# Optimization experiments

Measured on AMD Instinct MI355X. Metric: run time of the kernel, lower is better.

## Reference

```python
import jax, jax.numpy as jnp
import numpy as np

T_TOK, N_UNITS, E, H, L_PATH, N_PATHS, B, VOCAB = 16, 4096, 128, 128, 32, 1024, 8, 16384
MAX_PATH_LEN = 32
PAD_ID = 0


def _run_lstm(x, Wi, Wh, b):
    # x: [T, N, E]; torch gate order i, f, g, o
    Hh = Wh.shape[1]
    h0 = jnp.zeros((x.shape[1], Hh), x.dtype)
    def step(carry, xt):
        h, c = carry
        g = xt @ Wi.T + h @ Wh.T + b
        i, f, gg, o = jnp.split(g, 4, axis=-1)
        c = jax.nn.sigmoid(f) * c + jax.nn.sigmoid(i) * jnp.tanh(gg)
        h = jax.nn.sigmoid(o) * jnp.tanh(c)
        return (h, c), h
    _, ys = jax.lax.scan(step, (h0, h0), x)
    return ys


def _bilstm(x, lengths, Wif, Whf, bf, Wib, Whb, bb):
    # emulates pack_padded_sequence + bidirectional LSTM + pad_packed (zeros past length)
    T = x.shape[0]
    t = jnp.arange(T)[:, None]
    valid = t < lengths[None, :]
    out_f = _run_lstm(x, Wif, Whf, bf)
    rev = jnp.clip(lengths[None, :] - 1 - t, 0, T - 1)  # reverse within each valid prefix
    x_rev = jnp.take_along_axis(x, rev[:, :, None], axis=0)
    out_b = jnp.take_along_axis(_run_lstm(x_rev, Wib, Whb, bb), rev[:, :, None], axis=0)
    return jnp.concatenate([out_f, out_b], axis=-1) * valid[:, :, None]


def _layernorm(x, g, b):
    m = x.mean(-1, keepdims=True)
    v = ((x - m) ** 2).mean(-1, keepdims=True)
    return (x - m) * jax.lax.rsqrt(v + 1e-5) * g + b


def _forward(units, paths, unit_per_data, path_per_data, emb, tl_Wif, tl_Whf, tl_bf,
             tl_Wib, tl_Whb, tl_bb, lin_W, lin_b, ln_g, ln_b, attn_w, attn_b,
             pl_Wif, pl_Whf, pl_bf, pl_Wib, pl_Whb, pl_bb, ul_W, ul_b):
    # ---- _token_encoder ----
    is_pad = units == PAD_ID
    tok_len = jnp.where(is_pad.any(0), jnp.argmax(is_pad, 0), units.shape[0])
    x = emb[units]                                              # [T, NU, E]
    h = _bilstm(x, tok_len, tl_Wif, tl_Whf, tl_bf, tl_Wib, tl_Whb, tl_bb)  # [T, NU, 2H]
    out = h @ lin_W.T + lin_b                                   # [T, NU, E]
    q = jnp.tanh(_layernorm(out, ln_g, ln_b))
    scores = q @ attn_w.T + attn_b                              # [T, NU, 1] local attention
    scores = jnp.where(is_pad[:, :, None], -1e9, scores)
    w = jax.nn.softmax(scores, axis=0)
    tok_feat = jnp.einsum('tn,tne->ne', w[..., 0], out)         # [NU, E]
    # ---- _unit_to_path (vectorized ragged gather) ----
    Lp, Pn = paths.shape
    has_end = (paths == -1).any(0)
    fe = jnp.where(has_end, jnp.argmax(paths == -1, 0), Lp)
    ML = min(Lp, MAX_PATH_LEN)
    nb = unit_per_data.shape[0]
    data_of_path = jnp.repeat(jnp.arange(nb), path_per_data, total_repeat_length=Pn)
    u_off = jnp.cumsum(unit_per_data) - unit_per_data
    off_p = u_off[data_of_path]
    un_p = unit_per_data[data_of_path]
    pL = paths[:ML]
    t = jnp.arange(ML)[:, None]
    within = t < fe[None, :]
    keep = within & (pL >= 0) & (pL < un_p[None, :])
    gidx = jnp.clip(jnp.clip(pL, 0, None) + off_p[None, :], 0, tok_feat.shape[0] - 1)
    feats = tok_feat[gidx] * keep[:, :, None]                   # [ML, P, E]
    mask = jnp.where(within, (pL < 0) | (pL > un_p[None, :]), True)
    # ---- _path_encoder ----
    p_len = jnp.where(mask.any(0), jnp.argmax(mask, 0), ML)
    hp = _bilstm(feats, p_len, pl_Wif, pl_Whf, pl_bf, pl_Wib, pl_Whb, pl_bb)
    return hp @ ul_W.T + ul_b                                   # [ML, P, E]


def setup_inputs() -> dict:
    rng = np.random.default_rng(0)
    tok_len = rng.integers(4, T_TOK + 1, N_UNITS); tok_len[0] = T_TOK
    units = rng.integers(1, VOCAB, (T_TOK, N_UNITS))
    units = np.where(np.arange(T_TOK)[:, None] < tok_len[None, :], units, PAD_ID)
    upd = N_UNITS // B
    p_len = rng.integers(8, L_PATH + 1, N_PATHS); p_len[0] = L_PATH
    paths = rng.integers(0, upd, (L_PATH, N_PATHS))
    paths = np.where(np.arange(L_PATH)[:, None] < p_len[None, :], paths, -1)
    key = jax.random.key(0)
    ks = iter(jax.random.split(key, 24))
    def pn(shape, s=0.08):
        return (jax.random.normal(next(ks), shape) * s).astype(jnp.float32)
    return dict(
        units=jnp.asarray(units, jnp.int32),
        paths=jnp.asarray(paths, jnp.int32),
        unit_per_data=jnp.full((B,), upd, jnp.int32),
        path_per_data=jnp.full((B,), N_PATHS // B, jnp.int32),
        emb=pn((VOCAB, E)),
        tl_Wif=pn((4 * H, E)), tl_Whf=pn((4 * H, H)), tl_bf=pn((4 * H,)),
        tl_Wib=pn((4 * H, E)), tl_Whb=pn((4 * H, H)), tl_bb=pn((4 * H,)),
        lin_W=pn((E, 2 * H)), lin_b=pn((E,)),
        ln_g=jnp.ones((E,), jnp.float32), ln_b=jnp.zeros((E,), jnp.float32),
        attn_w=pn((1, E)), attn_b=pn((1,)),
        pl_Wif=pn((4 * H, E)), pl_Whf=pn((4 * H, H)), pl_bf=pn((4 * H,)),
        pl_Wib=pn((4 * H, E)), pl_Whb=pn((4 * H, H)), pl_bb=pn((4 * H,)),
        ul_W=pn((E, 2 * H)), ul_b=pn((E,)),
    )


def reference(units, paths, unit_per_data, path_per_data, emb, tl_Wif, tl_Whf, tl_bf,
              tl_Wib, tl_Whb, tl_bb, lin_W, lin_b, ln_g, ln_b, attn_w, attn_b,
              pl_Wif, pl_Whf, pl_bf, pl_Wib, pl_Whb, pl_bb, ul_W, ul_b):
    return _forward(units, paths, unit_per_data, path_per_data, emb, tl_Wif, tl_Whf, tl_bf,
                    tl_Wib, tl_Whb, tl_bb, lin_W, lin_b, ln_g, ln_b, attn_w, attn_b,
                    pl_Wif, pl_Whf, pl_bf, pl_Wib, pl_Whb, pl_bb, ul_W, ul_b)
```

## Files before the change

### kernel.cpp

```cpp
#include <hip/hip_runtime.h>
#include <cstdint>
#include <cstddef>

#define T_TOKN 16
#define NUNITS 4096
#define LPATH  32
#define NPATHS 1024
#define BNUM   8

typedef __attribute__((ext_vector_type(8))) short short8;
typedef __attribute__((ext_vector_type(4))) short short4x;
typedef __attribute__((ext_vector_type(4))) float f32x4;

enum : size_t {
  OFF_WFRAG   = 0,
  OFF_LINFRAG = 262144,
  OFF_OUTF    = 294912,
  OFF_OUTB    = OFF_OUTF + 4194304,
  OFF_OUTLIN  = OFF_OUTB + 4194304,
  OFF_SCORES  = OFF_OUTLIN + 8388608,
  OFF_TOKFEAT = OFF_SCORES + 65536,
  OFF_POUTF   = OFF_TOKFEAT + 524288,
  OFF_POUTB   = OFF_POUTF + 2097152,
  OFF_INT     = OFF_POUTB + 2097152,
  WS_FLOATS   = OFF_INT + 8192
};

static __device__ __forceinline__ unsigned short f2bf(float f) {
  union { float f; unsigned u; } v; v.f = f;
  unsigned r = v.u + 0x7fffu + ((v.u >> 16) & 1u);
  return (unsigned short)(r >> 16);
}
static __device__ __forceinline__ unsigned pack_bf(float a, float b) {
  return (unsigned)f2bf(a) | ((unsigned)f2bf(b) << 16);
}
static __device__ __forceinline__ float sigf(float x)      { return 1.f / (1.f + __expf(-x)); }
static __device__ __forceinline__ float tanhfast(float x)  { return 2.f / (1.f + __expf(-2.f * x)) - 1.f; }

__global__ void prep_kernel(
    const float* __restrict__ tWif, const float* __restrict__ tWhf,
    const float* __restrict__ tWib, const float* __restrict__ tWhb,
    const float* __restrict__ pWif, const float* __restrict__ pWhf,
    const float* __restrict__ pWib, const float* __restrict__ pWhb,
    const float* __restrict__ linW, const float* __restrict__ ulW,
    const int* __restrict__ units, const int* __restrict__ paths,
    const int* __restrict__ upd, const int* __restrict__ ppd,
    float* __restrict__ ws, int* __restrict__ ip)
{
  int idx = blockIdx.x * 256 + threadIdx.x;
  if (idx < 524288) {
    unsigned short* wf = (unsigned short*)(ws + OFF_WFRAG);
    int mat = idx >> 17, rem = idx & 131071;
    int i  = rem & 7;
    int lane = (rem >> 3) & 63;
    int ct = (rem >> 9) & 3;
    int ks = (rem >> 11) & 7;
    int wv = (rem >> 14) & 7;
    int g = wv * 64 + ct * 16 + (lane & 15);
    int k = ks * 32 + ((lane >> 4) << 3) + i;
    const float* Wi; const float* Wh;
    switch (mat) {
      case 0: Wi = tWif; Wh = tWhf; break;
      case 1: Wi = tWib; Wh = tWhb; break;
      case 2: Wi = pWif; Wh = pWhf; break;
      default: Wi = pWib; Wh = pWhb; break;
    }
    float v = (k < 128) ? Wi[g * 128 + k] : Wh[g * 128 + (k - 128)];
    wf[idx] = f2bf(v);
  } else if (idx < 524288 + 65536) {
    unsigned short* lf = (unsigned short*)(ws + OFF_LINFRAG);
    int i2 = idx - 524288;
    int mat = i2 >> 15, rem = i2 & 32767;
    int i  = rem & 7;
    int lane = (rem >> 3) & 63;
    int ks = (rem >> 9) & 7;
    int ct = (rem >> 12) & 7;
    int e = ct * 16 + (lane & 15);
    int k = ks * 32 + ((lane >> 4) << 3) + i;
    const float* W = mat ? ulW : linW;
    lf[i2] = f2bf(W[e * 256 + k]);
  } else if (idx < 589824 + 4096) {
    int n = idx - 589824;
    int len = T_TOKN;
    for (int t = 0; t < T_TOKN; ++t)
      if (units[t * NUNITS + n] == 0) { len = t; break; }
    ip[n] = len;
  } else if (idx < 589824 + 5120) {
    int p = idx - (589824 + 4096);
    int* fe_a  = ip + 4096;
    int* p_len = ip + 5120;
    int* off_p = ip + 6144;
    int* un_p  = ip + 7168;
    int cum = 0; int d = BNUM - 1;
    for (int dd = 0; dd < BNUM; ++dd) {
      int c2 = cum + ppd[dd];
      if (p < c2) { d = dd; break; }
      cum = c2;
    }
    int off = 0;
    for (int dd = 0; dd < d; ++dd) off += upd[dd];
    int un = upd[d];
    off_p[p] = off; un_p[p] = un;
    int f = LPATH;
    for (int t = 0; t < LPATH; ++t)
      if (paths[t * NPATHS + p] == -1) { f = t; break; }
    fe_a[p] = f;
    int pl = LPATH;
    for (int t = 0; t < LPATH; ++t) {
      int v = paths[t * NPATHS + p];
      if ((t >= f) || (v < 0) || (v > un)) { pl = t; break; }
    }
    p_len[p] = pl;
  }
}

template <int MODE>
__global__ __launch_bounds__(1024, 4) void lstm_kernel(
    const unsigned short* __restrict__ wfragAll,
    const float* __restrict__ biasF, const float* __restrict__ biasB,
    const float* __restrict__ src,
    const int* __restrict__ idxsrc,
    const int* __restrict__ lens,
    const int* __restrict__ fe_a, const int* __restrict__ off_p, const int* __restrict__ un_p,
    unsigned short* __restrict__ outF, unsigned short* __restrict__ outB)
{
  constexpr int NN   = MODE ? NPATHS : NUNITS;
  constexpr int TT   = MODE ? LPATH : T_TOKN;
  constexpr int M    = MODE ? 8 : 32;
  constexpr int MR   = MODE ? 16 : 32;
  constexpr int NRT  = MR / 16;
  constexpr int ASTR = 264;
  constexpr int GSTR = 514;

  __shared__ unsigned short ash[MR * ASTR];
  __shared__ float gates[MR * GSTR];

  int tid  = threadIdx.x;
  int dir  = blockIdx.y;
  int n0   = blockIdx.x * M;
  int lane = tid & 63, wv = tid >> 6;

  const unsigned short* wbase =
      wfragAll + (size_t)((MODE ? 2 : 0) + dir) * 131072;
  int wv8 = wv >> 1;
  short8 bfr[8][2];
#pragma unroll
  for (int ks = 0; ks < 8; ++ks)
#pragma unroll
    for (int c2 = 0; c2 < 2; ++c2) {
      int ct = ((wv & 1) << 1) | c2;
      bfr[ks][c2] = *(const short8*)&wbase[((((wv8 * 8 + ks) * 4 + ct) * 64) + lane) * 8];
    }

  if (MODE == 0) {
    for (int i = tid; i < MR * 128; i += 1024)
      ash[(i >> 7) * ASTR + 128 + (i & 127)] = 0;
  } else {
    for (int i = tid; i < MR * ASTR; i += 1024) ash[i] = 0;
  }

  const float* bcp = dir ? biasB : biasF;
  int j2 = MODE ? (tid & 127) : ((tid & 63) * 2);
  int ug = MODE ? (tid >> 7)  : (tid >> 6);
  float2 b2[4];
#pragma unroll
  for (int q = 0; q < 4; ++q) {
    if (MODE == 0) b2[q] = *(const float2*)&bcp[q * 128 + j2];
    else           b2[q] = make_float2(bcp[q * 128 + j2], 0.f);
  }
  constexpr int NU = MODE ? 1 : 2;
  float cst0[NU], cst1[NU];
  int   ulen[NU];
#pragma unroll
  for (int i = 0; i < NU; ++i) {
    cst0[i] = 0.f; cst1[i] = 0.f;
    ulen[i] = lens[n0 + ug * NU + i];
  }

  int gu, gk0;
  if (MODE == 0) { gu = tid >> 5; gk0 = (tid & 31) * 4; }
  else           { gu = tid >> 7; gk0 = tid & 127; }
  int gn = n0 + gu;
  int glen = lens[gn];
  int gfe = 0, goff = 0, gun = 0;
  if (MODE) { gfe = fe_a[gn]; goff = off_p[gn]; gun = un_p[gn]; }

  float4 xq; float xs;
  if (MODE == 0) {
    int tau = dir ? min(max(glen - 1, 0), TT - 1) : 0;
    int tok = idxsrc[tau * NN + gn];
    xq = *(const float4*)&src[(size_t)tok * 128 + gk0];
  } else {
    int tau = dir ? min(max(glen - 1, 0), TT - 1) : 0;
    int v = idxsrc[tau * NN + gn];
    bool keep = (tau < gfe) && (v >= 0) && (v < gun);
    xs = 0.f;
    if (keep) xs = src[(size_t)min(v + goff, NUNITS - 1) * 128 + gk0];
  }
  __syncthreads();

  for (int t = 0; t < TT; ++t) {
    if (MODE == 0) {
      short4x x4;
      x4[0] = (short)f2bf(xq.x); x4[1] = (short)f2bf(xq.y);
      x4[2] = (short)f2bf(xq.z); x4[3] = (short)f2bf(xq.w);
      *(short4x*)&ash[gu * ASTR + gk0] = x4;
    } else {
      ash[gu * ASTR + gk0] = f2bf(xs);
    }
    __syncthreads();

    {
      int tn = (t + 1 < TT) ? t + 1 : t;
      int taun = dir ? min(max(glen - 1 - tn, 0), TT - 1) : tn;
      int vn = idxsrc[taun * NN + gn];
      f32x4 acc[NRT][2];
#pragma unroll
      for (int rt = 0; rt < NRT; ++rt)
#pragma unroll
        for (int c2 = 0; c2 < 2; ++c2) {
          f32x4 z = {0.f, 0.f, 0.f, 0.f};
          acc[rt][c2] = z;
        }
#pragma unroll
      for (int ks = 0; ks < 8; ++ks) {
        short8 afr[NRT];
#pragma unroll
        for (int rt = 0; rt < NRT; ++rt)
          afr[rt] = *(const short8*)&ash[(rt * 16 + (lane & 15)) * ASTR + ks * 32 + ((lane >> 4) << 3)];
#pragma unroll
        for (int rt = 0; rt < NRT; ++rt)
#pragma unroll
          for (int c2 = 0; c2 < 2; ++c2)
            acc[rt][c2] = __builtin_amdgcn_mfma_f32_16x16x32_bf16(
                afr[rt], bfr[ks][c2], acc[rt][c2], 0, 0, 0);
      }
      if (MODE == 0) {
        xq = *(const float4*)&src[(size_t)vn * 128 + gk0];
      } else {
        bool keep = (taun < gfe) && (vn >= 0) && (vn < gun);
        xs = 0.f;
        if (keep) xs = src[(size_t)min(vn + goff, NUNITS - 1) * 128 + gk0];
      }
#pragma unroll
      for (int rt = 0; rt < NRT; ++rt)
#pragma unroll
        for (int c2 = 0; c2 < 2; ++c2) {
          int g = wv * 32 + c2 * 16 + (lane & 15);
#pragma unroll
          for (int r = 0; r < 4; ++r) {
            int u = rt * 16 + ((lane >> 4) << 2) + r;
            gates[u * GSTR + g] = acc[rt][c2][r];
          }
        }
    }
    __syncthreads();

#pragma unroll
    for (int i = 0; i < NU; ++i) {
      int u = ug * NU + i;
      int n = n0 + u;
      if (MODE == 0) {
        float2 g0 = *(const float2*)&gates[u * GSTR + j2];
        float2 g1 = *(const float2*)&gates[u * GSTR + 128 + j2];
        float2 g2 = *(const float2*)&gates[u * GSTR + 256 + j2];
        float2 g3 = *(const float2*)&gates[u * GSTR + 384 + j2];
        float i0 = sigf(g0.x + b2[0].x), i1 = sigf(g0.y + b2[0].y);
        float f0 = sigf(g1.x + b2[1].x), f1 = sigf(g1.y + b2[1].y);
        float c0 = tanhfast(g2.x + b2[2].x), c1 = tanhfast(g2.y + b2[2].y);
        float o0 = sigf(g3.x + b2[3].x), o1 = sigf(g3.y + b2[3].y);
        float cA = f0 * cst0[i] + i0 * c0;
        float cB = f1 * cst1[i] + i1 * c1;
        cst0[i] = cA; cst1[i] = cB;
        float h0 = o0 * tanhfast(cA);
        float h1 = o1 * tanhfast(cB);
        unsigned hp = pack_bf(h0, h1);
        *(unsigned*)&ash[u * ASTR + 128 + j2] = hp;
        if (dir == 0) {
          *(unsigned*)&outF[((size_t)t * NN + n) * 128 + j2] = hp;
        } else {
          int L = ulen[i];
          if (t < L) *(unsigned*)&outB[((size_t)(L - 1 - t) * NN + n) * 128 + j2] = hp;
          else       *(unsigned*)&outB[((size_t)t * NN + n) * 128 + j2] = 0;
        }
      } else {
        float p0 = gates[u * GSTR + j2]       + b2[0].x;
        float p1 = gates[u * GSTR + 128 + j2] + b2[1].x;
        float p2 = gates[u * GSTR + 256 + j2] + b2[2].x;
        float p3 = gates[u * GSTR + 384 + j2] + b2[3].x;
        float ig = sigf(p0), fg = sigf(p1), gg = tanhfast(p2), og = sigf(p3);
        float c = fg * cst0[i] + ig * gg;
        cst0[i] = c;
        float h = og * tanhfast(c);
        unsigned short hb = f2bf(h);
        ash[u * ASTR + 128 + j2] = hb;
        if (dir == 0) {
          outF[((size_t)t * NN + n) * 128 + j2] = hb;
        } else {
          int L = ulen[i];
          if (t < L) outB[((size_t)(L - 1 - t) * NN + n) * 128 + j2] = hb;
          else       outB[((size_t)t * NN + n) * 128 + j2] = 0;
        }
      }
    }
  }
}

template <int EPI>
__global__ __launch_bounds__(256) void gemm_mfma(
    const unsigned short* __restrict__ INf, const unsigned short* __restrict__ INb,
    const int* __restrict__ lens,
    const unsigned short* __restrict__ Bfrag, const float* __restrict__ bias,
    float* __restrict__ OUT, float* __restrict__ scores,
    const float* __restrict__ lng, const float* __restrict__ lnb,
    const float* __restrict__ attw, const float* __restrict__ attb,
    const int* __restrict__ units, int Nn)
{
  constexpr int OSTR = 132;
  __shared__ float outs[64 * OSTR];
  __shared__ float red1[256];
  __shared__ float red2[256];
  __shared__ float rowm[64], rowr[64];
  __shared__ float awsh[128], lgsh[128], lbsh[128];

  int tid = threadIdx.x, lane = tid & 63, wv = tid >> 6;
  int row0 = blockIdx.x * 64;
  int t = row0 / Nn, n0 = row0 % Nn;

  if (EPI == 1 && tid < 128) {
    awsh[tid] = attw[tid]; lgsh[tid] = lng[tid]; lbsh[tid] = lnb[tid];
  }

  short8 bfr[8][2];
#pragma unroll
  for (int ks = 0; ks < 8; ++ks)
#pragma unroll
    for (int c2 = 0; c2 < 2; ++c2) {
      int ct = wv * 2 + c2;
      bfr[ks][c2] = *(const short8*)&Bfrag[(((ct * 8 + ks) * 64) + lane) * 8];
    }

  int rb = lane & 15;
  int koq = (lane >> 4) << 3;
  bool val[4];
#pragma unroll
  for (int rt = 0; rt < 4; ++rt)
    val[rt] = (EPI == 1) ? true : (t < lens[n0 + rt * 16 + rb]);

  f32x4 acc[4][2];
#pragma unroll
  for (int rt = 0; rt < 4; ++rt)
#pragma unroll
    for (int c2 = 0; c2 < 2; ++c2) {
      f32x4 z = {0.f, 0.f, 0.f, 0.f};
      acc[rt][c2] = z;
    }

#pragma unroll
  for (int ks = 0; ks < 8; ++ks) {
    const unsigned short* P = (ks < 4) ? INf : INb;
    int koff = (ks & 3) * 32 + koq;
#pragma unroll
    for (int rt = 0; rt < 4; ++rt) {
      short8 a = {0, 0, 0, 0, 0, 0, 0, 0};
      if (val[rt])
        a = *(const short8*)&P[((size_t)(row0 + rt * 16 + rb)) * 128 + koff];
#pragma unroll
      for (int c2 = 0; c2 < 2; ++c2)
        acc[rt][c2] = __builtin_amdgcn_mfma_f32_16x16x32_bf16(
            a, bfr[ks][c2], acc[rt][c2], 0, 0, 0);
    }
  }

  float bc[2];
#pragma unroll
  for (int c2 = 0; c2 < 2; ++c2) bc[c2] = bias[wv * 32 + c2 * 16 + rb];
#pragma unroll
  for (int rt = 0; rt < 4; ++rt)
#pragma unroll
    for (int c2 = 0; c2 < 2; ++c2) {
      int col = wv * 32 + c2 * 16 + rb;
      int ub  = rt * 16 + ((lane >> 4) << 2);
#pragma unroll
      for (int r = 0; r < 4; ++r)
        outs[(ub + r) * OSTR + col] = acc[rt][c2][r] + bc[c2];
    }
  __syncthreads();

  int row = tid >> 2, seg = tid & 3;
  const float* rp = &outs[row * OSTR + seg * 32];
  size_t go = ((size_t)(row0 + row)) * 128 + seg * 32;

  if (EPI == 0) {
#pragma unroll
    for (int x = 0; x < 8; ++x)
      *(f32x4*)&OUT[go + x * 4] = *(const f32x4*)&rp[x * 4];
  } else {
    f32x4 v[8];
    float s = 0.f, s2 = 0.f;
#pragma unroll
    for (int x = 0; x < 8; ++x) {
      v[x] = *(const f32x4*)&rp[x * 4];
#pragma unroll
      for (int c = 0; c < 4; ++c) { s += v[x][c]; s2 += v[x][c] * v[x][c]; }
    }
    red1[tid] = s; red2[tid] = s2;
    __syncthreads();
    if (tid < 64) {
      float a = red1[tid * 4] + red1[tid * 4 + 1] + red1[tid * 4 + 2] + red1[tid * 4 + 3];
      float b = red2[tid * 4] + red2[tid * 4 + 1] + red2[tid * 4 + 2] + red2[tid * 4 + 3];
      float m = a * (1.f / 128.f);
      float var = b * (1.f / 128.f) - m * m;
      rowm[tid] = m;
      rowr[tid] = rsqrtf(var + 1e-5f);
    }
    __syncthreads();
    float m = rowm[row], rs = rowr[row];
    float sp = 0.f;
#pragma unroll
    for (int x = 0; x < 8; ++x) {
#pragma unroll
      for (int c = 0; c < 4; ++c) {
        int col = seg * 32 + x * 4 + c;
        float q = tanhfast((v[x][c] - m) * rs * lgsh[col] + lbsh[col]);
        sp += q * awsh[col];
      }
      *(f32x4*)&OUT[go + x * 4] = v[x];
    }
    red1[tid] = sp;
    __syncthreads();
    if (tid < 64) {
      float s3 = red1[tid * 4] + red1[tid * 4 + 1] + red1[tid * 4 + 2] + red1[tid * 4 + 3]
               + attb[0];
      int n = n0 + tid;
      if (units[t * NUNITS + n] == 0) s3 = -1e9f;
      scores[t * NUNITS + n] = s3;
    }
  }
}

__global__ __launch_bounds__(128) void softmax_feat_kernel(
    const float* __restrict__ scores, const float* __restrict__ out_lin,
    float* __restrict__ tok_feat)
{
  int n = blockIdx.x;
  int e = threadIdx.x;
  float s[T_TOKN];
  float m = -1e30f;
#pragma unroll
  for (int t = 0; t < T_TOKN; ++t) { s[t] = scores[t * NUNITS + n]; m = fmaxf(m, s[t]); }
  float sum = 0.f;
#pragma unroll
  for (int t = 0; t < T_TOKN; ++t) { s[t] = expf(s[t] - m); sum += s[t]; }
  float inv = 1.f / sum;
  float a = 0.f;
#pragma unroll
  for (int t = 0; t < T_TOKN; ++t)
    a += s[t] * inv * out_lin[((size_t)t * NUNITS + n) * 128 + e];
  tok_feat[n * 128 + e] = a;
}

extern "C" void kernel_launch(void* const* d_in, const int* in_sizes, int n_in,
                              void* d_out, int out_size, void* d_ws, size_t ws_size,
                              hipStream_t stream)
{
  const int*   units = (const int*)d_in[0];
  const int*   paths = (const int*)d_in[1];
  const int*   upd   = (const int*)d_in[2];
  const int*   ppd   = (const int*)d_in[3];
  const float* emb   = (const float*)d_in[4];
  const float* tWif  = (const float*)d_in[5];
  const float* tWhf  = (const float*)d_in[6];
  const float* tbf   = (const float*)d_in[7];
  const float* tWib  = (const float*)d_in[8];
  const float* tWhb  = (const float*)d_in[9];
  const float* tbb   = (const float*)d_in[10];
  const float* linW  = (const float*)d_in[11];
  const float* linb  = (const float*)d_in[12];
  const float* lng   = (const float*)d_in[13];
  const float* lnb   = (const float*)d_in[14];
  const float* attw  = (const float*)d_in[15];
  const float* attb  = (const float*)d_in[16];
  const float* pWif  = (const float*)d_in[17];
  const float* pWhf  = (const float*)d_in[18];
  const float* pbf   = (const float*)d_in[19];
  const float* pWib  = (const float*)d_in[20];
  const float* pWhb  = (const float*)d_in[21];
  const float* pbb   = (const float*)d_in[22];
  const float* ulW   = (const float*)d_in[23];
  const float* ulb   = (const float*)d_in[24];

  float* ws = (float*)d_ws;
  int*   ip = (int*)(ws + OFF_INT);
  if (ws_size < WS_FLOATS * sizeof(float)) return;

  unsigned short* wfrag   = (unsigned short*)(ws + OFF_WFRAG);
  unsigned short* linfrag = (unsigned short*)(ws + OFF_LINFRAG);
  unsigned short* ulfrag  = linfrag + 32768;
  unsigned short* OUTF  = (unsigned short*)(ws + OFF_OUTF);
  unsigned short* OUTB  = (unsigned short*)(ws + OFF_OUTB);
  unsigned short* POUTF = (unsigned short*)(ws + OFF_POUTF);
  unsigned short* POUTB = (unsigned short*)(ws + OFF_POUTB);

  prep_kernel<<<2324, 256, 0, stream>>>(tWif, tWhf, tWib, tWhb,
                                        pWif, pWhf, pWib, pWhb,
                                        linW, ulW, units, paths, upd, ppd,
                                        ws, ip);

  lstm_kernel<0><<<dim3(128, 2), 1024, 0, stream>>>(
      wfrag, tbf, tbb, emb, units, ip , nullptr, nullptr, nullptr,
      OUTF, OUTB);

  gemm_mfma<1><<<1024, 256, 0, stream>>>(
      OUTF, OUTB, ip , linfrag, linb,
      ws + OFF_OUTLIN, ws + OFF_SCORES, lng, lnb, attw, attb, units, NUNITS);

  softmax_feat_kernel<<<4096, 128, 0, stream>>>(ws + OFF_SCORES, ws + OFF_OUTLIN,
                                                ws + OFF_TOKFEAT);

  lstm_kernel<1><<<dim3(128, 2), 1024, 0, stream>>>(
      wfrag, pbf, pbb, ws + OFF_TOKFEAT, paths, ip + 5120 ,
      ip + 4096 , ip + 6144 , ip + 7168 ,
      POUTF, POUTB);

  gemm_mfma<0><<<512, 256, 0, stream>>>(
      POUTF, POUTB, ip + 5120 , ulfrag, ulb,
      (float*)d_out, nullptr, nullptr, nullptr, nullptr, nullptr, nullptr, NPATHS);
}
```

Measured before the change: 322.2 us.

## Ping-pong two row groups in LSTM so pointwise overlaps the other group's MFMA

The LSTM recurrence kernel now splits each block's rows into two independent groups of 16 with double-buffered shared A-tiles and gate buffers. The MFMA step for one group is interleaved with the pointwise gate update of the other, so each barrier phase mixes matrix and elementwise work instead of running them serially. It also skips the gate math for padded timesteps and just writes zeros. The cost is more complex control flow and extra shared memory. Mode 1 now leaves half its threads idle in the pointwise phase and clamps the path index.

```diff
diff --git a/kernel.cpp b/kernel.cpp
--- a/kernel.cpp
+++ b/kernel.cpp
@@ -9,7 +9,6 @@
 #define BNUM   8
 
 typedef __attribute__((ext_vector_type(8))) short short8;
-typedef __attribute__((ext_vector_type(4))) short short4x;
 typedef __attribute__((ext_vector_type(4))) float f32x4;
 
 enum : size_t {
@@ -126,19 +125,18 @@
 {
   constexpr int NN   = MODE ? NPATHS : NUNITS;
   constexpr int TT   = MODE ? LPATH : T_TOKN;
-  constexpr int M    = MODE ? 8 : 32;
-  constexpr int MR   = MODE ? 16 : 32;
-  constexpr int NRT  = MR / 16;
+  constexpr int GR   = MODE ? 4 : 16;
   constexpr int ASTR = 264;
   constexpr int GSTR = 514;
 
-  __shared__ unsigned short ash[MR * ASTR];
-  __shared__ float gates[MR * GSTR];
+  __shared__ unsigned short ash[2][16 * ASTR];
+  __shared__ float gates[2][16 * GSTR];
 
   int tid  = threadIdx.x;
   int dir  = blockIdx.y;
-  int n0   = blockIdx.x * M;
+  int n0   = blockIdx.x * (2 * GR);
   int lane = tid & 63, wv = tid >> 6;
+  int koq  = (lane >> 4) << 3;
 
   const unsigned short* wbase =
       wfragAll + (size_t)((MODE ? 2 : 0) + dir) * 131072;
@@ -152,158 +150,163 @@
       bfr[ks][c2] = *(const short8*)&wbase[((((wv8 * 8 + ks) * 4 + ct) * 64) + lane) * 8];
     }
 
-  if (MODE == 0) {
-    for (int i = tid; i < MR * 128; i += 1024)
-      ash[(i >> 7) * ASTR + 128 + (i & 127)] = 0;
-  } else {
-    for (int i = tid; i < MR * ASTR; i += 1024) ash[i] = 0;
+  for (int i = tid; i < 2 * 16 * ASTR / 2; i += 1024) ((unsigned*)ash)[i] = 0u;
+
+  int j2 = MODE ? (tid & 127) : (lane * 2);
+  int ug = MODE ? (tid >> 7) : (tid >> 6);
+
+  int nn[2], ulen[2];
+  int gfe[2] = {0, 0}, goff[2] = {0, 0}, gun[2] = {0, 0};
+#pragma unroll
+  for (int g = 0; g < 2; ++g) {
+    int n = n0 + g * GR + ug;
+    if constexpr (MODE) n = min(n, NPATHS - 1);
+    nn[g] = n; ulen[g] = lens[n];
+    if constexpr (MODE) { gfe[g] = fe_a[n]; goff[g] = off_p[n]; gun[g] = un_p[n]; }
   }
 
   const float* bcp = dir ? biasB : biasF;
-  int j2 = MODE ? (tid & 127) : ((tid & 63) * 2);
-  int ug = MODE ? (tid >> 7)  : (tid >> 6);
   float2 b2[4];
 #pragma unroll
   for (int q = 0; q < 4; ++q) {
-    if (MODE == 0) b2[q] = *(const float2*)&bcp[q * 128 + j2];
-    else           b2[q] = make_float2(bcp[q * 128 + j2], 0.f);
-  }
-  constexpr int NU = MODE ? 1 : 2;
-  float cst0[NU], cst1[NU];
-  int   ulen[NU];
-#pragma unroll
-  for (int i = 0; i < NU; ++i) {
-    cst0[i] = 0.f; cst1[i] = 0.f;
-    ulen[i] = lens[n0 + ug * NU + i];
-  }
-
-  int gu, gk0;
-  if (MODE == 0) { gu = tid >> 5; gk0 = (tid & 31) * 4; }
-  else           { gu = tid >> 7; gk0 = tid & 127; }
-  int gn = n0 + gu;
-  int glen = lens[gn];
-  int gfe = 0, goff = 0, gun = 0;
-  if (MODE) { gfe = fe_a[gn]; goff = off_p[gn]; gun = un_p[gn]; }
-
-  float4 xq; float xs;
-  if (MODE == 0) {
-    int tau = dir ? min(max(glen - 1, 0), TT - 1) : 0;
-    int tok = idxsrc[tau * NN + gn];
-    xq = *(const float4*)&src[(size_t)tok * 128 + gk0];
-  } else {
-    int tau = dir ? min(max(glen - 1, 0), TT - 1) : 0;
-    int v = idxsrc[tau * NN + gn];
-    bool keep = (tau < gfe) && (v >= 0) && (v < gun);
-    xs = 0.f;
-    if (keep) xs = src[(size_t)min(v + goff, NUNITS - 1) * 128 + gk0];
-  }
+    if constexpr (MODE == 0) b2[q] = *(const float2*)&bcp[q * 128 + j2];
+    else                     b2[q] = make_float2(bcp[q * 128 + j2], 0.f);
+  }
+
+  float cst0[2] = {0.f, 0.f}, cst1[2] = {0.f, 0.f};
+  float2 xq2[2];
+  float  xq1[2];
+  (void)xq2; (void)xq1; (void)cst1;
+
+#define XLOAD(GG, TN) do {                                                    \
+    int tc = min((TN), TT - 1);                                               \
+    if constexpr (MODE == 0) {                                                \
+      int tau = dir ? min(max(ulen[GG] - 1 - tc, 0), TT - 1) : tc;            \
+      int tok = idxsrc[tau * NN + nn[GG]];                                    \
+      xq2[GG] = *(const float2*)&src[(size_t)tok * 128 + j2];                 \
+    } else {                                                                  \
+      if (ug < GR) {                                                          \
+        int tau = dir ? min(max(ulen[GG] - 1 - tc, 0), TT - 1) : tc;          \
+        int v = idxsrc[tau * NN + nn[GG]];                                    \
+        bool keep = (tau < gfe[GG]) && (v >= 0) && (v < gun[GG]);             \
+        float xv = 0.f;                                                       \
+        if (keep) xv = src[(size_t)min(v + goff[GG], NUNITS - 1) * 128 + j2]; \
+        xq1[GG] = xv;                                                         \
+      }                                                                       \
+    }                                                                         \
+  } while (0)
+
+#define XWRITE(GG) do {                                                       \
+    if constexpr (MODE == 0)                                                  \
+      *(unsigned*)&ash[GG][ug * ASTR + j2] = pack_bf(xq2[GG].x, xq2[GG].y);   \
+    else if (ug < GR)                                                         \
+      ash[GG][ug * ASTR + j2] = f2bf(xq1[GG]);                                \
+  } while (0)
+
+#define GSTORE(GG, P0, P1) do {                                               \
+    int col = wv * 32 + (lane & 15);                                          \
+    int ub  = (lane >> 4) << 2;                                               \
+    float* gg = gates[GG];                                                    \
+    for (int r = 0; r < 4; ++r) {                                             \
+      gg[(ub + r) * GSTR + col]      = (P0)[r];                               \
+      gg[(ub + r) * GSTR + col + 16] = (P1)[r];                               \
+    }                                                                         \
+  } while (0)
+
+#define POINTWISE(GG, TPW) do {                                               \
+    int tpw = (TPW);                                                          \
+    if constexpr (MODE == 0) {                                                \
+      int L = ulen[GG]; int n = nn[GG];                                       \
+      if (tpw < L) {                                 \
+        const float* gg = gates[GG] + ug * GSTR + j2;                         \
+        float2 g0 = *(const float2*)(gg);                                     \
+        float2 g1 = *(const float2*)(gg + 128);                               \
+        float2 g2 = *(const float2*)(gg + 256);                               \
+        float2 g3 = *(const float2*)(gg + 384);                               \
+        float i0 = sigf(g0.x + b2[0].x), i1 = sigf(g0.y + b2[0].y);           \
+        float f0 = sigf(g1.x + b2[1].x), f1 = sigf(g1.y + b2[1].y);           \
+        float c0 = tanhfast(g2.x + b2[2].x), c1 = tanhfast(g2.y + b2[2].y);   \
+        float o0 = sigf(g3.x + b2[3].x), o1 = sigf(g3.y + b2[3].y);           \
+        float cA = f0 * cst0[GG] + i0 * c0;                                   \
+        float cB = f1 * cst1[GG] + i1 * c1;                                   \
+        cst0[GG] = cA; cst1[GG] = cB;                                         \
+        unsigned hp = pack_bf(o0 * tanhfast(cA), o1 * tanhfast(cB));          \
+        *(unsigned*)&ash[GG][ug * ASTR + 128 + j2] = hp;                      \
+        if (dir == 0)                                                         \
+          *(unsigned*)&outF[((size_t)tpw * NN + n) * 128 + j2] = hp;          \
+        else                                                                  \
+          *(unsigned*)&outB[((size_t)(L - 1 - tpw) * NN + n) * 128 + j2] = hp;\
+      } else {                 \
+        if (dir == 0)                                                         \
+          *(unsigned*)&outF[((size_t)tpw * NN + n) * 128 + j2] = 0u;          \
+        else                                                                  \
+          *(unsigned*)&outB[((size_t)tpw * NN + n) * 128 + j2] = 0u;          \
+      }                                                                       \
+    } else if (ug < GR) {                                                     \
+      int L = ulen[GG]; int n = nn[GG];                                       \
+      if (tpw < L) {                                                          \
+        const float* gg = gates[GG] + ug * GSTR + j2;                         \
+        float p0 = gg[0]   + b2[0].x;                                         \
+        float p1 = gg[128] + b2[1].x;                                         \
+        float p2 = gg[256] + b2[2].x;                                         \
+        float p3 = gg[384] + b2[3].x;                                         \
+        float c = sigf(p1) * cst0[GG] + sigf(p0) * tanhfast(p2);              \
+        cst0[GG] = c;                                                         \
+        unsigned short hb = f2bf(sigf(p3) * tanhfast(c));                     \
+        ash[GG][ug * ASTR + 128 + j2] = hb;                                   \
+        if (dir == 0) outF[((size_t)tpw * NN + n) * 128 + j2] = hb;           \
+        else          outB[((size_t)(L - 1 - tpw) * NN + n) * 128 + j2] = hb; \
+      } else {                                                                \
+        if (dir == 0) outF[((size_t)tpw * NN + n) * 128 + j2] = 0;            \
+        else          outB[((size_t)tpw * NN + n) * 128 + j2] = 0;            \
+      }                                                                       \
+    }                                                                         \
+  } while (0)
+
   __syncthreads();
-
+  XLOAD(0, 0);
+  XLOAD(1, 0);
+  XWRITE(0);
+  __syncthreads();
+
+#pragma unroll 1
   for (int t = 0; t < TT; ++t) {
-    if (MODE == 0) {
-      short4x x4;
-      x4[0] = (short)f2bf(xq.x); x4[1] = (short)f2bf(xq.y);
-      x4[2] = (short)f2bf(xq.z); x4[3] = (short)f2bf(xq.w);
-      *(short4x*)&ash[gu * ASTR + gk0] = x4;
-    } else {
-      ash[gu * ASTR + gk0] = f2bf(xs);
+    {
+      f32x4 p0 = {0.f, 0.f, 0.f, 0.f}, p1 = {0.f, 0.f, 0.f, 0.f};
+#pragma unroll
+      for (int ks = 0; ks < 8; ++ks) {
+        short8 a = *(const short8*)&ash[0][(lane & 15) * ASTR + ks * 32 + koq];
+        p0 = __builtin_amdgcn_mfma_f32_16x16x32_bf16(a, bfr[ks][0], p0, 0, 0, 0);
+        p1 = __builtin_amdgcn_mfma_f32_16x16x32_bf16(a, bfr[ks][1], p1, 0, 0, 0);
+      }
+      XWRITE(1);
+      if (t + 1 < TT) XLOAD(0, t + 1);
+      if (t > 0) POINTWISE(1, t - 1);
+      GSTORE(0, p0, p1);
     }
     __syncthreads();
 
     {
-      int tn = (t + 1 < TT) ? t + 1 : t;
-      int taun = dir ? min(max(glen - 1 - tn, 0), TT - 1) : tn;
-      int vn = idxsrc[taun * NN + gn];
-      f32x4 acc[NRT][2];
-#pragma unroll
-      for (int rt = 0; rt < NRT; ++rt)
-#pragma unroll
-        for (int c2 = 0; c2 < 2; ++c2) {
-          f32x4 z = {0.f, 0.f, 0.f, 0.f};
-          acc[rt][c2] = z;
-        }
+      f32x4 p0 = {0.f, 0.f, 0.f, 0.f}, p1 = {0.f, 0.f, 0.f, 0.f};
 #pragma unroll
       for (int ks = 0; ks < 8; ++ks) {
-        short8 afr[NRT];
-#pragma unroll
-        for (int rt = 0; rt < NRT; ++rt)
-          afr[rt] = *(const short8*)&ash[(rt * 16 + (lane & 15)) * ASTR + ks * 32 + ((lane >> 4) << 3)];
-#pragma unroll
-        for (int rt = 0; rt < NRT; ++rt)
-#pragma unroll
-          for (int c2 = 0; c2 < 2; ++c2)
-            acc[rt][c2] = __builtin_amdgcn_mfma_f32_16x16x32_bf16(
-                afr[rt], bfr[ks][c2], acc[rt][c2], 0, 0, 0);
+        short8 a = *(const short8*)&ash[1][(lane & 15) * ASTR + ks * 32 + koq];
+        p0 = __builtin_amdgcn_mfma_f32_16x16x32_bf16(a, bfr[ks][0], p0, 0, 0, 0);
+        p1 = __builtin_amdgcn_mfma_f32_16x16x32_bf16(a, bfr[ks][1], p1, 0, 0, 0);
       }
-      if (MODE == 0) {
-        xq = *(const float4*)&src[(size_t)vn * 128 + gk0];
-      } else {
-        bool keep = (taun < gfe) && (vn >= 0) && (vn < gun);
-        xs = 0.f;
-        if (keep) xs = src[(size_t)min(vn + goff, NUNITS - 1) * 128 + gk0];
-      }
-#pragma unroll
-      for (int rt = 0; rt < NRT; ++rt)
-#pragma unroll
-        for (int c2 = 0; c2 < 2; ++c2) {
-          int g = wv * 32 + c2 * 16 + (lane & 15);
-#pragma unroll
-          for (int r = 0; r < 4; ++r) {
-            int u = rt * 16 + ((lane >> 4) << 2) + r;
-            gates[u * GSTR + g] = acc[rt][c2][r];
-          }
-        }
+      if (t + 1 < TT) XWRITE(0);
+      if (t + 1 < TT) XLOAD(1, t + 1);
+      POINTWISE(0, t);
+      GSTORE(1, p0, p1);
     }
     __syncthreads();
-
-#pragma unroll
-    for (int i = 0; i < NU; ++i) {
-      int u = ug * NU + i;
-      int n = n0 + u;
-      if (MODE == 0) {
-        float2 g0 = *(const float2*)&gates[u * GSTR + j2];
-        float2 g1 = *(const float2*)&gates[u * GSTR + 128 + j2];
-        float2 g2 = *(const float2*)&gates[u * GSTR + 256 + j2];
-        float2 g3 = *(const float2*)&gates[u * GSTR + 384 + j2];
-        float i0 = sigf(g0.x + b2[0].x), i1 = sigf(g0.y + b2[0].y);
-        float f0 = sigf(g1.x + b2[1].x), f1 = sigf(g1.y + b2[1].y);
-        float c0 = tanhfast(g2.x + b2[2].x), c1 = tanhfast(g2.y + b2[2].y);
-        float o0 = sigf(g3.x + b2[3].x), o1 = sigf(g3.y + b2[3].y);
-        float cA = f0 * cst0[i] + i0 * c0;
-        float cB = f1 * cst1[i] + i1 * c1;
-        cst0[i] = cA; cst1[i] = cB;
-        float h0 = o0 * tanhfast(cA);
-        float h1 = o1 * tanhfast(cB);
-        unsigned hp = pack_bf(h0, h1);
-        *(unsigned*)&ash[u * ASTR + 128 + j2] = hp;
-        if (dir == 0) {
-          *(unsigned*)&outF[((size_t)t * NN + n) * 128 + j2] = hp;
-        } else {
-          int L = ulen[i];
-          if (t < L) *(unsigned*)&outB[((size_t)(L - 1 - t) * NN + n) * 128 + j2] = hp;
-          else       *(unsigned*)&outB[((size_t)t * NN + n) * 128 + j2] = 0;
-        }
-      } else {
-        float p0 = gates[u * GSTR + j2]       + b2[0].x;
-        float p1 = gates[u * GSTR + 128 + j2] + b2[1].x;
-        float p2 = gates[u * GSTR + 256 + j2] + b2[2].x;
-        float p3 = gates[u * GSTR + 384 + j2] + b2[3].x;
-        float ig = sigf(p0), fg = sigf(p1), gg = tanhfast(p2), og = sigf(p3);
-        float c = fg * cst0[i] + ig * gg;
-        cst0[i] = c;
-        float h = og * tanhfast(c);
-        unsigned short hb = f2bf(h);
-        ash[u * ASTR + 128 + j2] = hb;
-        if (dir == 0) {
-          outF[((size_t)t * NN + n) * 128 + j2] = hb;
-        } else {
-          int L = ulen[i];
-          if (t < L) outB[((size_t)(L - 1 - t) * NN + n) * 128 + j2] = hb;
-          else       outB[((size_t)t * NN + n) * 128 + j2] = 0;
-        }
-      }
-    }
-  }
+  }
+  POINTWISE(1, TT - 1);
+
+#undef XLOAD
+#undef XWRITE
+#undef GSTORE
+#undef POINTWISE
 }
 
 template <int EPI>
```

After: 330.7 us. +2.6%, slower.

## Restructure LSTM step loop: cache indices, defer stores, drop a barrier

Applied to the files above, without the earlier changes.

Loads the per-block token/path index table into shared memory once instead of reading global memory each step. Moves the next input's bf16 write to the end of the step so only one block barrier per timestep is needed. Defers each step's hidden-state global store to the following iteration so it overlaps with the MFMA work. Skips gate computation for timesteps past a sequence's length and emits zeros there instead. This adds shared memory and register state, and relies on padded outputs being masked downstream.

```diff
diff --git a/kernel.cpp b/kernel.cpp
--- a/kernel.cpp
+++ b/kernel.cpp
@@ -134,6 +134,7 @@
 
   __shared__ unsigned short ash[MR * ASTR];
   __shared__ float gates[MR * GSTR];
+  __shared__ int   idxL[M * TT];
 
   int tid  = threadIdx.x;
   int dir  = blockIdx.y;
@@ -158,6 +159,10 @@
   } else {
     for (int i = tid; i < MR * ASTR; i += 1024) ash[i] = 0;
   }
+  for (int i = tid; i < M * TT; i += 1024) {
+    int u = i / TT, tt = i - u * TT;
+    idxL[i] = idxsrc[tt * NN + (n0 + u)];
+  }
 
   const float* bcp = dir ? biasB : biasF;
   int j2 = MODE ? (tid & 127) : ((tid & 63) * 2);
@@ -171,10 +176,12 @@
   constexpr int NU = MODE ? 1 : 2;
   float cst0[NU], cst1[NU];
   int   ulen[NU];
+  unsigned hp_prev[NU];
 #pragma unroll
   for (int i = 0; i < NU; ++i) {
     cst0[i] = 0.f; cst1[i] = 0.f;
     ulen[i] = lens[n0 + ug * NU + i];
+    hp_prev[i] = 0u;
   }
 
   int gu, gk0;
@@ -186,34 +193,66 @@
   if (MODE) { gfe = fe_a[gn]; goff = off_p[gn]; gun = un_p[gn]; }
 
   float4 xq; float xs;
+  __syncthreads();
+
+  {
+    int tau = dir ? min(max(glen - 1, 0), TT - 1) : 0;
+    int v = idxL[gu * TT + tau];
+    if (MODE == 0) {
+      xq = *(const float4*)&src[(size_t)v * 128 + gk0];
+    } else {
+      bool keep = (tau < gfe) && (v >= 0) && (v < gun);
+      xs = keep ? src[(size_t)min(v + goff, NUNITS - 1) * 128 + gk0] : 0.f;
+    }
+  }
   if (MODE == 0) {
-    int tau = dir ? min(max(glen - 1, 0), TT - 1) : 0;
-    int tok = idxsrc[tau * NN + gn];
-    xq = *(const float4*)&src[(size_t)tok * 128 + gk0];
+    short4x x4;
+    x4[0] = (short)f2bf(xq.x); x4[1] = (short)f2bf(xq.y);
+    x4[2] = (short)f2bf(xq.z); x4[3] = (short)f2bf(xq.w);
+    *(short4x*)&ash[gu * ASTR + gk0] = x4;
   } else {
-    int tau = dir ? min(max(glen - 1, 0), TT - 1) : 0;
-    int v = idxsrc[tau * NN + gn];
-    bool keep = (tau < gfe) && (v >= 0) && (v < gun);
-    xs = 0.f;
-    if (keep) xs = src[(size_t)min(v + goff, NUNITS - 1) * 128 + gk0];
+    ash[gu * ASTR + gk0] = f2bf(xs);
   }
   __syncthreads();
 
+#pragma unroll 1
   for (int t = 0; t < TT; ++t) {
-    if (MODE == 0) {
-      short4x x4;
-      x4[0] = (short)f2bf(xq.x); x4[1] = (short)f2bf(xq.y);
-      x4[2] = (short)f2bf(xq.z); x4[3] = (short)f2bf(xq.w);
-      *(short4x*)&ash[gu * ASTR + gk0] = x4;
-    } else {
-      ash[gu * ASTR + gk0] = f2bf(xs);
-    }
-    __syncthreads();
-
+    if (t > 0) {
+      int tpw = t - 1;
+#pragma unroll
+      for (int i = 0; i < NU; ++i) {
+        int u = ug * NU + i, n = n0 + u, L = ulen[i];
+        bool vld = tpw < L;
+        if (MODE == 0) {
+          if (dir == 0) {
+            *(unsigned*)&outF[((size_t)tpw * NN + n) * 128 + j2] = hp_prev[i];
+          } else {
+            size_t tr = vld ? (size_t)(L - 1 - tpw) : (size_t)tpw;
+            *(unsigned*)&outB[(tr * NN + n) * 128 + j2] = vld ? hp_prev[i] : 0u;
+          }
+        } else {
+          unsigned short hb = (unsigned short)hp_prev[i];
+          if (dir == 0) {
+            outF[((size_t)tpw * NN + n) * 128 + j2] = hb;
+          } else {
+            size_t tr = vld ? (size_t)(L - 1 - tpw) : (size_t)tpw;
+            outB[(tr * NN + n) * 128 + j2] = vld ? hb : (unsigned short)0;
+          }
+        }
+      }
+    }
     {
       int tn = (t + 1 < TT) ? t + 1 : t;
       int taun = dir ? min(max(glen - 1 - tn, 0), TT - 1) : tn;
-      int vn = idxsrc[taun * NN + gn];
+      int vn = idxL[gu * TT + taun];
+      if (MODE == 0) {
+        xq = *(const float4*)&src[(size_t)vn * 128 + gk0];
+      } else {
+        bool keep = (taun < gfe) && (vn >= 0) && (vn < gun);
+        xs = keep ? src[(size_t)min(vn + goff, NUNITS - 1) * 128 + gk0] : 0.f;
+      }
+    }
+    {
       f32x4 acc[NRT][2];
 #pragma unroll
       for (int rt = 0; rt < NRT; ++rt)
@@ -234,13 +273,6 @@
           for (int c2 = 0; c2 < 2; ++c2)
             acc[rt][c2] = __builtin_amdgcn_mfma_f32_16x16x32_bf16(
                 afr[rt], bfr[ks][c2], acc[rt][c2], 0, 0, 0);
-      }
-      if (MODE == 0) {
-        xq = *(const float4*)&src[(size_t)vn * 128 + gk0];
-      } else {
-        bool keep = (taun < gfe) && (vn >= 0) && (vn < gun);
-        xs = 0.f;
-        if (keep) xs = src[(size_t)min(vn + goff, NUNITS - 1) * 128 + gk0];
       }
 #pragma unroll
       for (int rt = 0; rt < NRT; ++rt)
@@ -259,47 +291,72 @@
 #pragma unroll
     for (int i = 0; i < NU; ++i) {
       int u = ug * NU + i;
-      int n = n0 + u;
-      if (MODE == 0) {
-        float2 g0 = *(const float2*)&gates[u * GSTR + j2];
-        float2 g1 = *(const float2*)&gates[u * GSTR + 128 + j2];
-        float2 g2 = *(const float2*)&gates[u * GSTR + 256 + j2];
-        float2 g3 = *(const float2*)&gates[u * GSTR + 384 + j2];
-        float i0 = sigf(g0.x + b2[0].x), i1 = sigf(g0.y + b2[0].y);
-        float f0 = sigf(g1.x + b2[1].x), f1 = sigf(g1.y + b2[1].y);
-        float c0 = tanhfast(g2.x + b2[2].x), c1 = tanhfast(g2.y + b2[2].y);
-        float o0 = sigf(g3.x + b2[3].x), o1 = sigf(g3.y + b2[3].y);
-        float cA = f0 * cst0[i] + i0 * c0;
-        float cB = f1 * cst1[i] + i1 * c1;
-        cst0[i] = cA; cst1[i] = cB;
-        float h0 = o0 * tanhfast(cA);
-        float h1 = o1 * tanhfast(cB);
-        unsigned hp = pack_bf(h0, h1);
-        *(unsigned*)&ash[u * ASTR + 128 + j2] = hp;
-        if (dir == 0) {
-          *(unsigned*)&outF[((size_t)t * NN + n) * 128 + j2] = hp;
+      int L = ulen[i];
+      if (t < L) {
+        if (MODE == 0) {
+          float2 g0 = *(const float2*)&gates[u * GSTR + j2];
+          float2 g1 = *(const float2*)&gates[u * GSTR + 128 + j2];
+          float2 g2 = *(const float2*)&gates[u * GSTR + 256 + j2];
+          float2 g3 = *(const float2*)&gates[u * GSTR + 384 + j2];
+          float i0 = sigf(g0.x + b2[0].x), i1 = sigf(g0.y + b2[0].y);
+          float f0 = sigf(g1.x + b2[1].x), f1 = sigf(g1.y + b2[1].y);
+          float c0 = tanhfast(g2.x + b2[2].x), c1 = tanhfast(g2.y + b2[2].y);
+          float o0 = sigf(g3.x + b2[3].x), o1 = sigf(g3.y + b2[3].y);
+          float cA = f0 * cst0[i] + i0 * c0;
+          float cB = f1 * cst1[i] + i1 * c1;
+          cst0[i] = cA; cst1[i] = cB;
+          unsigned hp = pack_bf(o0 * tanhfast(cA), o1 * tanhfast(cB));
+          *(unsigned*)&ash[u * ASTR + 128 + j2] = hp;
+          hp_prev[i] = hp;
         } else {
-          int L = ulen[i];
-          if (t < L) *(unsigned*)&outB[((size_t)(L - 1 - t) * NN + n) * 128 + j2] = hp;
-          else       *(unsigned*)&outB[((size_t)t * NN + n) * 128 + j2] = 0;
+          float p0 = gates[u * GSTR + j2]       + b2[0].x;
+          float p1 = gates[u * GSTR + 128 + j2] + b2[1].x;
+          float p2 = gates[u * GSTR + 256 + j2] + b2[2].x;
+          float p3 = gates[u * GSTR + 384 + j2] + b2[3].x;
+          float ig = sigf(p0), fg = sigf(p1), gg = tanhfast(p2), og = sigf(p3);
+          float c = fg * cst0[i] + ig * gg;
+          cst0[i] = c;
+          unsigned short hb = f2bf(og * tanhfast(c));
+          ash[u * ASTR + 128 + j2] = hb;
+          hp_prev[i] = (unsigned)hb;
         }
       } else {
-        float p0 = gates[u * GSTR + j2]       + b2[0].x;
-        float p1 = gates[u * GSTR + 128 + j2] + b2[1].x;
-        float p2 = gates[u * GSTR + 256 + j2] + b2[2].x;
-        float p3 = gates[u * GSTR + 384 + j2] + b2[3].x;
-        float ig = sigf(p0), fg = sigf(p1), gg = tanhfast(p2), og = sigf(p3);
-        float c = fg * cst0[i] + ig * gg;
-        cst0[i] = c;
-        float h = og * tanhfast(c);
-        unsigned short hb = f2bf(h);
-        ash[u * ASTR + 128 + j2] = hb;
+        hp_prev[i] = 0u;
+      }
+    }
+    if (t + 1 < TT) {
+      if (MODE == 0) {
+        short4x x4;
+        x4[0] = (short)f2bf(xq.x); x4[1] = (short)f2bf(xq.y);
+        x4[2] = (short)f2bf(xq.z); x4[3] = (short)f2bf(xq.w);
+        *(short4x*)&ash[gu * ASTR + gk0] = x4;
+      } else {
+        ash[gu * ASTR + gk0] = f2bf(xs);
+      }
+    }
+    __syncthreads();
+  }
+
+  {
+    int tpw = TT - 1;
+#pragma unroll
+    for (int i = 0; i < NU; ++i) {
+      int u = ug * NU + i, n = n0 + u, L = ulen[i];
+      bool vld = tpw < L;
+      if (MODE == 0) {
         if (dir == 0) {
-          outF[((size_t)t * NN + n) * 128 + j2] = hb;
+          *(unsigned*)&outF[((size_t)tpw * NN + n) * 128 + j2] = hp_prev[i];
         } else {
-          int L = ulen[i];
-          if (t < L) outB[((size_t)(L - 1 - t) * NN + n) * 128 + j2] = hb;
-          else       outB[((size_t)t * NN + n) * 128 + j2] = 0;
+          size_t tr = vld ? (size_t)(L - 1 - tpw) : (size_t)tpw;
+          *(unsigned*)&outB[(tr * NN + n) * 128 + j2] = vld ? hp_prev[i] : 0u;
+        }
+      } else {
+        unsigned short hb = (unsigned short)hp_prev[i];
+        if (dir == 0) {
+          outF[((size_t)tpw * NN + n) * 128 + j2] = hb;
+        } else {
+          size_t tr = vld ? (size_t)(L - 1 - tpw) : (size_t)tpw;
+          outB[(tr * NN + n) * 128 + j2] = vld ? hb : (unsigned short)0;
         }
       }
     }
```

New measurement: 317.7 us. No clear change (-1.4%).
